# Kernel tuning notes

Hardware: AMD Instinct MI355X
Metric: run time of the kernel (lower is better)

The kernel has to match this reference:

```python
import jax, jax.numpy as jnp
import numpy as np

K = 4
G = 64
IN_DIM = 256
OUT_DIM = 256
BATCH = 512
T0, T1 = -1.0, 1.0


def setup_inputs() -> dict:
    key = jax.random.key(0)
    kx, kw = jax.random.split(key)
    x = jax.random.uniform(kx, (BATCH, IN_DIM), jnp.float32, T0, T1)
    # xavier_normal_ on [G+K, in, out]: std = sqrt(2 / (fan_in + fan_out)) with fan over last two dims
    std = (2.0 / (IN_DIM + OUT_DIM)) ** 0.5
    w = jax.random.normal(kw, (G + K, IN_DIM, OUT_DIM), jnp.float32) * std
    # knot vector: k-1 repeats of t0, linspace(t0,t1,G+1), k-1 repeats of t1
    t = jnp.concatenate([
        jnp.full((K - 1,), T0, jnp.float32),
        jnp.linspace(T0, T1, G + 1, dtype=jnp.float32),
        jnp.full((K - 1,), T1, jnp.float32),
    ])
    return {"x": x, "w": w, "t": t, "k": K}


def _basis(x, t, k):
    """Cox-de Boor: the k nonzero order-k B-spline basis values at each x.
    Returns (idx, N): idx [..., k] basis indices i-k+1..i, N [..., k] values."""
    n_t = t.shape[0]
    # interval i with t[i] <= x < t[i+1], clipped to the valid span
    i = jnp.clip(jnp.searchsorted(t, x, side='right') - 1, k - 1, n_t - k - 1)
    N = jnp.ones(x.shape + (1,), x.dtype)
    for p in range(1, k):  # static small loop (k=4)
        jj = jnp.arange(1, p + 1)
        left = x[..., None] - t[i[..., None] + 1 - jj]   # [..., p]
        right = t[i[..., None] + jj] - x[..., None]      # [..., p]
        saved = jnp.zeros_like(x)
        vals = []
        for r in range(p):
            d = right[..., r] + left[..., p - 1 - r]      # t[i+r+1] - t[i+r+1-p]
            temp = N[..., r] / d
            vals.append(saved + right[..., r] * temp)
            saved = left[..., p - 1 - r] * temp
        vals.append(saved)
        N = jnp.stack(vals, -1)
    idx = i[..., None] - (k - 1) + jnp.arange(k)
    return idx, N


def reference(x, w, t, k):
    in_dim = x.shape[1]
    n_rows = w.shape[0]
    idx, y1 = _basis(x, t, k)                             # [B,in,k], [B,in,k]
    # last row of w (index -1 == n_rows-1) weights the SiLU residual term
    idx_full = jnp.concatenate(
        [idx, jnp.full(idx.shape[:-1] + (1,), n_rows - 1, idx.dtype)], -1)  # [B,in,k+1]
    silu = x * jax.nn.sigmoid(x)
    y2 = jnp.concatenate([y1, silu[..., None]], -1)       # [B,in,k+1]
    # gather local spline coefficients: w2[b,c,j,o] = w[idx_full[b,c,j], c, o]
    w2 = w[idx_full, jnp.arange(in_dim)[None, :, None], :]  # [B,in,k+1,out]
    return jnp.einsum('bcjo,bcj->bo', w2, y2)             # [B,out]
```

## Files before the change

kernel.cpp:

```cpp
#include <hip/hip_runtime.h>
#include <math.h>
#include <stdint.h>

#define IN_DIM  256
#define OUT_DIM 256
#define NROWS   68
#define NT      71
#define BATCH   512
#define W_ELEMS (NROWS * IN_DIM * OUT_DIM)
#define PART_FLOATS (8 * BATCH * OUT_DIM)

__device__ __forceinline__ uint32_t bf16_rne(float f) {
  uint32_t u = __builtin_bit_cast(uint32_t, f);
  return (u + 0x7fffu + ((u >> 16) & 1u)) >> 16;
}

__global__ __launch_bounds__(256) void cvt_kernel(const float* __restrict__ w,
                                                  uint32_t* __restrict__ wb) {
  const int base = (blockIdx.x * 256 + threadIdx.x) * 8;
  const float4 a = *(const float4*)(w + base);
  const float4 b = *(const float4*)(w + base + 4);
  uint4 o;
  o.x = bf16_rne(a.x) | (bf16_rne(a.y) << 16);
  o.y = bf16_rne(a.z) | (bf16_rne(a.w) << 16);
  o.z = bf16_rne(b.x) | (bf16_rne(b.y) << 16);
  o.w = bf16_rne(b.z) | (bf16_rne(b.w) << 16);
  *(uint4*)(wb + base / 2) = o;
}

__device__ __forceinline__ void fma8(const uint4 q, const float y, float* acc) {
  acc[0] += y * __builtin_bit_cast(float, q.x << 16);
  acc[1] += y * __builtin_bit_cast(float, q.x & 0xffff0000u);
  acc[2] += y * __builtin_bit_cast(float, q.y << 16);
  acc[3] += y * __builtin_bit_cast(float, q.y & 0xffff0000u);
  acc[4] += y * __builtin_bit_cast(float, q.z << 16);
  acc[5] += y * __builtin_bit_cast(float, q.z & 0xffff0000u);
  acc[6] += y * __builtin_bit_cast(float, q.w << 16);
  acc[7] += y * __builtin_bit_cast(float, q.w & 0xffff0000u);
}

__global__ __launch_bounds__(256, 4) void kan_gather_kernel(
    const float* __restrict__ x, const uint4* __restrict__ wp,
    const float* __restrict__ t, float* __restrict__ part) {
  __shared__ float  lt[NT];
  __shared__ float4 nA[32][4];
  __shared__ float  sA[32][4];
  __shared__ int    bA[32][4];
  __shared__ float  red[4][1024];

  const int tid = threadIdx.x;
  const unsigned bid = blockIdx.x;
  const int cchunk = bid & 7;
  const int bgroup = bid >> 3;

  if (tid < NT) lt[tid] = t[tid];
  __syncthreads();

  if (tid < 128) {
    const int bb = tid >> 5;
    const int cl = tid & 31;
    const float xv = x[(size_t)(bgroup * 4 + bb) * IN_DIM + cchunk * 32 + cl];
    int i = 3 + (int)floorf((xv + 1.0f) * 32.0f);
    i = i < 3 ? 3 : (i > 66 ? 66 : i);
    while (i > 3 && xv < lt[i]) --i;
    while (i < 66 && xv >= lt[i + 1]) ++i;

    float N0 = 1.f, N1 = 0.f, N2 = 0.f, N3 = 0.f;
    {
      const float l1 = xv - lt[i];
      const float r1 = lt[i + 1] - xv;
      const float tp = N0 / (r1 + l1);
      N1 = l1 * tp; N0 = r1 * tp;
    }
    {
      const float l1 = xv - lt[i];
      const float l2 = xv - lt[i - 1];
      const float r1 = lt[i + 1] - xv;
      const float r2 = lt[i + 2] - xv;
      float saved = 0.f;
      const float tp0 = N0 / (r1 + l2);
      const float n0 = saved + r1 * tp0; saved = l2 * tp0;
      const float tp1 = N1 / (r2 + l1);
      const float n1 = saved + r2 * tp1; saved = l1 * tp1;
      N0 = n0; N1 = n1; N2 = saved;
    }
    {
      const float l1 = xv - lt[i];
      const float l2 = xv - lt[i - 1];
      const float l3 = xv - lt[i - 2];
      const float r1 = lt[i + 1] - xv;
      const float r2 = lt[i + 2] - xv;
      const float r3 = lt[i + 3] - xv;
      float saved = 0.f;
      const float tp0 = N0 / (r1 + l3);
      const float n0 = saved + r1 * tp0; saved = l3 * tp0;
      const float tp1 = N1 / (r2 + l2);
      const float n1 = saved + r2 * tp1; saved = l2 * tp1;
      const float tp2 = N2 / (r3 + l1);
      const float n2 = saved + r3 * tp2; saved = l1 * tp2;
      N0 = n0; N1 = n1; N2 = n2; N3 = saved;
    }
    nA[cl][bb] = make_float4(N0, N1, N2, N3);
    sA[cl][bb] = xv / (1.0f + expf(-xv));
    bA[cl][bb] = i - 3;
  }
  __syncthreads();

  const int wv   = tid >> 6;
  const int lane = tid & 63;
  const int half = lane >> 5;
  const int ol   = lane & 31;

  float acc[4][8];
  #pragma unroll
  for (int b = 0; b < 4; ++b) {
    #pragma unroll
    for (int j = 0; j < 8; ++j) acc[b][j] = 0.f;
  }

  for (int pp = 0; pp < 4; ++pp) {
    const int cl = wv * 8 + pp * 2 + half;
    const uint32_t cbase = (uint32_t)((cchunk * 32 + cl) * 32 + ol);
    const uint4 q4 = wp[cbase + 67u * 8192u];
    #pragma unroll
    for (int b = 0; b < 4; ++b) {
      const float4 yv = nA[cl][b];
      const float  ys = sA[cl][b];
      const uint32_t rb = cbase + ((uint32_t)bA[cl][b] << 13);
      const uint4 q0 = wp[rb];
      const uint4 q1 = wp[rb +  8192u];
      const uint4 q2 = wp[rb + 16384u];
      const uint4 q3 = wp[rb + 24576u];
      fma8(q0, yv.x, acc[b]);
      fma8(q1, yv.y, acc[b]);
      fma8(q2, yv.z, acc[b]);
      fma8(q3, yv.w, acc[b]);
      fma8(q4, ys,   acc[b]);
    }
  }

  #pragma unroll
  for (int b = 0; b < 4; ++b) {
    #pragma unroll
    for (int j = 0; j < 8; ++j)
      acc[b][j] += __shfl_xor(acc[b][j], 32, 64);
  }

  if (half == 0) {
    #pragma unroll
    for (int b = 0; b < 4; ++b) {
      #pragma unroll
      for (int j = 0; j < 8; ++j)
        red[wv][b * 256 + ol * 8 + j] = acc[b][j];
    }
  }
  __syncthreads();

  {
    const int b  = tid >> 6;
    const int o4 = tid & 63;
    const float4 a0 = *(const float4*)&red[0][b * 256 + o4 * 4];
    const float4 a1 = *(const float4*)&red[1][b * 256 + o4 * 4];
    const float4 a2 = *(const float4*)&red[2][b * 256 + o4 * 4];
    const float4 a3 = *(const float4*)&red[3][b * 256 + o4 * 4];
    float4 s;
    s.x = (a0.x + a1.x) + (a2.x + a3.x);
    s.y = (a0.y + a1.y) + (a2.y + a3.y);
    s.z = (a0.z + a1.z) + (a2.z + a3.z);
    s.w = (a0.w + a1.w) + (a2.w + a3.w);
    *(float4*)(part + ((size_t)cchunk * BATCH + bgroup * 4 + b) * OUT_DIM + o4 * 4) = s;
  }
}

__global__ __launch_bounds__(256) void reduce_kernel(const float* __restrict__ part,
                                                     float* __restrict__ out) {
  const int q = blockIdx.x * 256 + threadIdx.x;
  const int S = BATCH * OUT_DIM / 4;
  const float4* p = (const float4*)part;
  float4 s = p[q];
  #pragma unroll
  for (int k = 1; k < 8; ++k) {
    const float4 a = p[q + k * S];
    s.x += a.x; s.y += a.y; s.z += a.z; s.w += a.w;
  }
  ((float4*)out)[q] = s;
}

extern "C" void kernel_launch(void* const* d_in, const int* in_sizes, int n_in,
                              void* d_out, int out_size, void* d_ws, size_t ws_size,
                              hipStream_t stream) {
  const float* x = (const float*)d_in[0];
  const float* w = (const float*)d_in[1];
  const float* t = (const float*)d_in[2];
  float* out  = (float*)d_out;
  float* part = (float*)d_ws;
  uint32_t* wb = (uint32_t*)d_ws + PART_FLOATS;
  cvt_kernel<<<W_ELEMS / (256 * 8), 256, 0, stream>>>(w, wb);
  kan_gather_kernel<<<1024, 256, 0, stream>>>(x, (const uint4*)wb, t, part);
  reduce_kernel<<<BATCH * OUT_DIM / 4 / 256, 256, 0, stream>>>(part, out);
}
```

Before: 98.15 us.

## Stage per-channel bf16 weight slabs in LDS via global_load_lds for batch reuse

Each block now covers 32 batch rows and 16 input channels. For each channel it copies all 68 bf16 weight rows of that channel into LDS with direct global-to-LDS loads, then gathers the spline coefficients for 32 batch rows from LDS instead of from global memory. This is meant to cut redundant scattered global reads of the weights. In exchange the grid shrinks to 256 blocks, each channel step waits on a barrier with no double buffering, and the partial buffer doubles to 16 slices, which adds work to the reduce kernel.

```diff
diff --git a/kernel.cpp b/kernel.cpp
--- a/kernel.cpp
+++ b/kernel.cpp
@@ -8,7 +8,8 @@
 #define NT      71
 #define BATCH   512
 #define W_ELEMS (NROWS * IN_DIM * OUT_DIM)
-#define PART_FLOATS (8 * BATCH * OUT_DIM)
+#define NCG     16
+#define PART_FLOATS (NCG * BATCH * OUT_DIM)
 
 __device__ __forceinline__ uint32_t bf16_rne(float f) {
   uint32_t u = __builtin_bit_cast(uint32_t, f);
@@ -39,27 +40,27 @@
   acc[7] += y * __builtin_bit_cast(float, q.w & 0xffff0000u);
 }
 
-__global__ __launch_bounds__(256, 4) void kan_gather_kernel(
+__global__ __launch_bounds__(256) void kan_gather_kernel(
     const float* __restrict__ x, const uint4* __restrict__ wp,
     const float* __restrict__ t, float* __restrict__ part) {
   __shared__ float  lt[NT];
-  __shared__ float4 nA[32][4];
-  __shared__ float  sA[32][4];
-  __shared__ int    bA[32][4];
-  __shared__ float  red[4][1024];
+  __shared__ float4 nA[16][32];
+  __shared__ float  sA[16][32];
+  __shared__ int    bA[16][32];
+  __shared__ uint4  lbuf[NROWS * 32];
 
   const int tid = threadIdx.x;
   const unsigned bid = blockIdx.x;
-  const int cchunk = bid & 7;
-  const int bgroup = bid >> 3;
+  const int cg     = bid & 15;
+  const int bgroup = bid >> 4;
 
   if (tid < NT) lt[tid] = t[tid];
   __syncthreads();
 
-  if (tid < 128) {
-    const int bb = tid >> 5;
-    const int cl = tid & 31;
-    const float xv = x[(size_t)(bgroup * 4 + bb) * IN_DIM + cchunk * 32 + cl];
+  for (int p = tid; p < 512; p += 256) {
+    const int cl = p >> 5;
+    const int bb = p & 31;
+    const float xv = x[(size_t)(bgroup * 32 + bb) * IN_DIM + cg * 16 + cl];
     int i = 3 + (int)floorf((xv + 1.0f) * 32.0f);
     i = i < 3 ? 3 : (i > 66 ? 66 : i);
     while (i > 3 && xv < lt[i]) --i;
@@ -113,62 +114,54 @@
 
   float acc[4][8];
   #pragma unroll
-  for (int b = 0; b < 4; ++b) {
+  for (int bp = 0; bp < 4; ++bp) {
     #pragma unroll
-    for (int j = 0; j < 8; ++j) acc[b][j] = 0.f;
+    for (int j = 0; j < 8; ++j) acc[bp][j] = 0.f;
   }
 
-  for (int pp = 0; pp < 4; ++pp) {
-    const int cl = wv * 8 + pp * 2 + half;
-    const uint32_t cbase = (uint32_t)((cchunk * 32 + cl) * 32 + ol);
-    const uint4 q4 = wp[cbase + 67u * 8192u];
+  for (int ch = 0; ch < 16; ++ch) {
+    {
+      const uint32_t cb = (uint32_t)(cg * 16 + ch) * 32;
+      for (int i = wv; i < 34; i += 4) {
+        const int Xu = i * 64 + lane;
+        const int r  = Xu >> 5;
+        const int off = Xu & 31;
+        const uint4* src = wp + ((uint32_t)r << 13) + cb + off;
+        __builtin_amdgcn_global_load_lds((const uint32_t*)src,
+                                         (uint32_t*)&lbuf[i * 64], 16, 0, 0);
+      }
+    }
+    __syncthreads();
+
+    const uint4 q4 = lbuf[67 * 32 + ol];
     #pragma unroll
-    for (int b = 0; b < 4; ++b) {
-      const float4 yv = nA[cl][b];
-      const float  ys = sA[cl][b];
-      const uint32_t rb = cbase + ((uint32_t)bA[cl][b] << 13);
-      const uint4 q0 = wp[rb];
-      const uint4 q1 = wp[rb +  8192u];
-      const uint4 q2 = wp[rb + 16384u];
-      const uint4 q3 = wp[rb + 24576u];
-      fma8(q0, yv.x, acc[b]);
-      fma8(q1, yv.y, acc[b]);
-      fma8(q2, yv.z, acc[b]);
-      fma8(q3, yv.w, acc[b]);
-      fma8(q4, ys,   acc[b]);
+    for (int bp = 0; bp < 4; ++bp) {
+      const int bb = wv * 8 + bp * 2 + half;
+      const float4 yv = nA[ch][bb];
+      const float  ys = sA[ch][bb];
+      const int    rb = bA[ch][bb] * 32 + ol;
+      const uint4 q0 = lbuf[rb];
+      const uint4 q1 = lbuf[rb + 32];
+      const uint4 q2 = lbuf[rb + 64];
+      const uint4 q3 = lbuf[rb + 96];
+      fma8(q0, yv.x, acc[bp]);
+      fma8(q1, yv.y, acc[bp]);
+      fma8(q2, yv.z, acc[bp]);
+      fma8(q3, yv.w, acc[bp]);
+      fma8(q4, ys,   acc[bp]);
     }
+    __syncthreads();
   }
 
-  #pragma unroll
-  for (int b = 0; b < 4; ++b) {
+  {
+    float* dst = part + ((size_t)cg * BATCH + bgroup * 32) * OUT_DIM;
     #pragma unroll
-    for (int j = 0; j < 8; ++j)
-      acc[b][j] += __shfl_xor(acc[b][j], 32, 64);
-  }
-
-  if (half == 0) {
-    #pragma unroll
-    for (int b = 0; b < 4; ++b) {
-      #pragma unroll
-      for (int j = 0; j < 8; ++j)
-        red[wv][b * 256 + ol * 8 + j] = acc[b][j];
+    for (int bp = 0; bp < 4; ++bp) {
+      const int bb = wv * 8 + bp * 2 + half;
+      float* d = dst + (size_t)bb * OUT_DIM + ol * 8;
+      *(float4*)d       = make_float4(acc[bp][0], acc[bp][1], acc[bp][2], acc[bp][3]);
+      *(float4*)(d + 4) = make_float4(acc[bp][4], acc[bp][5], acc[bp][6], acc[bp][7]);
     }
-  }
-  __syncthreads();
-
-  {
-    const int b  = tid >> 6;
-    const int o4 = tid & 63;
-    const float4 a0 = *(const float4*)&red[0][b * 256 + o4 * 4];
-    const float4 a1 = *(const float4*)&red[1][b * 256 + o4 * 4];
-    const float4 a2 = *(const float4*)&red[2][b * 256 + o4 * 4];
-    const float4 a3 = *(const float4*)&red[3][b * 256 + o4 * 4];
-    float4 s;
-    s.x = (a0.x + a1.x) + (a2.x + a3.x);
-    s.y = (a0.y + a1.y) + (a2.y + a3.y);
-    s.z = (a0.z + a1.z) + (a2.z + a3.z);
-    s.w = (a0.w + a1.w) + (a2.w + a3.w);
-    *(float4*)(part + ((size_t)cchunk * BATCH + bgroup * 4 + b) * OUT_DIM + o4 * 4) = s;
   }
 }
 
@@ -179,7 +172,7 @@
   const float4* p = (const float4*)part;
   float4 s = p[q];
   #pragma unroll
-  for (int k = 1; k < 8; ++k) {
+  for (int k = 1; k < NCG; ++k) {
     const float4 a = p[q + k * S];
     s.x += a.x; s.y += a.y; s.z += a.z; s.w += a.w;
   }
@@ -196,6 +189,6 @@
   float* part = (float*)d_ws;
   uint32_t* wb = (uint32_t*)d_ws + PART_FLOATS;
   cvt_kernel<<<W_ELEMS / (256 * 8), 256, 0, stream>>>(w, wb);
-  kan_gather_kernel<<<1024, 256, 0, stream>>>(x, (const uint4*)wb, t, part);
+  kan_gather_kernel<<<256, 256, 0, stream>>>(x, (const uint4*)wb, t, part);
   reduce_kernel<<<BATCH * OUT_DIM / 4 / 256, 256, 0, stream>>>(part, out);
 }
```

After: 100.5 us. 2.4% more time.
